# Kernel tuning notes

Measured on AMD Instinct MI355X. Metric: run time of the kernel, lower is better.

The kernel has to match this reference:

```python
import jax, jax.numpy as jnp
import numpy as np

B, T, D = 4, 2048, 1024
E, K, F = 8, 2, 4096


def setup_inputs() -> dict:
    key = jax.random.key(0)
    ks = jax.random.split(key, 6)
    s = 0.02
    return {
        "x": jax.random.normal(ks[0], (B, T, D), dtype=jnp.float32),
        "gate_w": jax.random.normal(ks[1], (D, E), dtype=jnp.float32) * s,
        "w1": jax.random.normal(ks[2], (E, D, F), dtype=jnp.float32) * s,
        "b1": jax.random.normal(ks[3], (E, F), dtype=jnp.float32) * s,
        "w2": jax.random.normal(ks[4], (E, F, D), dtype=jnp.float32) * s,
        "b2": jax.random.normal(ks[5], (E, D), dtype=jnp.float32) * s,
    }


def reference(x, gate_w, w1, b1, w2, b2):
    b, t, d = x.shape
    xf = x.reshape(-1, d)                       # [N, D]
    logits = xf @ gate_w                        # [N, E]
    topv, topi = jax.lax.top_k(logits, K)       # [N, K]
    gates = jax.nn.softmax(topv, axis=-1)       # [N, K]
    # per-token per-expert combine weight (zero for unselected experts)
    onehot = jax.nn.one_hot(topi, E, dtype=xf.dtype)       # [N, K, E]
    comb = jnp.einsum('nk,nke->ne', gates, onehot)          # [N, E]
    out = jnp.zeros_like(xf)
    for e in range(E):  # small fixed expert loop; keeps [N,F] intermediate only
        h = jax.nn.gelu(xf @ w1[e] + b1[e], approximate=False)  # [N, F]
        y = h @ w2[e] + b2[e]                                   # [N, D]
        out = out + comb[:, e:e + 1] * y
    return out.reshape(b, t, d)
```

## Files before the change

kernel.cpp:

```cpp
#include <hip/hip_runtime.h>
#include <stdint.h>
#include <stddef.h>

#define N_TOK 8192
#define DIM   1024
#define NE    8
#define NF    4096
#define TM    128
#define TN    128
#define BKK   64
#define RCAP  (N_TOK*2 + NE*TM)
#define MAXMT (N_TOK/TM)

typedef __attribute__((ext_vector_type(8))) short short8;
typedef __attribute__((ext_vector_type(4))) float f32x4;

__device__ __forceinline__ float bf2f(short s){
  unsigned u = ((unsigned)(unsigned short)s) << 16;
  return __builtin_bit_cast(float, u);
}
__device__ __forceinline__ short f2bf(float f){
  unsigned u = __builtin_bit_cast(unsigned, f);
  u += 0x7fffu + ((u >> 16) & 1u);
  return (short)(u >> 16);
}

#define GLD_LDS16(g, l) __builtin_amdgcn_global_load_lds( \
    (const __attribute__((address_space(1))) void*)(g),   \
    (__attribute__((address_space(3))) void*)(l), 16, 0, 0)

__global__ __launch_bounds__(256) void gate_kernel(
    const float* __restrict__ x, const float* __restrict__ gw,
    int* __restrict__ topi, float* __restrict__ gatev, int* __restrict__ ctrl)
{
  int t = blockIdx.x * 4 + (threadIdx.x >> 6);
  int lane = threadIdx.x & 63;
  const float* xr = x + (size_t)t * DIM;
  float p[NE];
  #pragma unroll
  for (int e = 0; e < NE; e++) p[e] = 0.f;
  for (int i = lane; i < DIM; i += 64){
    float xv = xr[i];
    const float* g = gw + i * NE;
    #pragma unroll
    for (int e = 0; e < NE; e++) p[e] += xv * g[e];
  }
  #pragma unroll
  for (int off = 32; off > 0; off >>= 1){
    #pragma unroll
    for (int e = 0; e < NE; e++) p[e] += __shfl_xor(p[e], off, 64);
  }
  if (lane == 0){
    int i1 = 0; float v1 = p[0];
    #pragma unroll
    for (int e = 1; e < NE; e++) if (p[e] > v1){ v1 = p[e]; i1 = e; }
    int i2 = -1; float v2 = -3.4e38f;
    #pragma unroll
    for (int e = 0; e < NE; e++) if (e != i1 && p[e] > v2){ v2 = p[e]; i2 = e; }
    float ex = expf(v2 - v1);
    float g2 = ex / (1.f + ex);
    float g1 = 1.f - g2;
    topi[t*2]   = i1;  topi[t*2+1]  = i2;
    gatev[t*2]  = g1;  gatev[t*2+1] = g2;
    atomicAdd(&ctrl[i1], 1);
    atomicAdd(&ctrl[i2], 1);
  }
}

__global__ void scan_kernel(int* ctrl){
  if (threadIdx.x == 0){
    int tot = 0;
    for (int e = 0; e < NE; e++){
      int c = ctrl[e];
      int cap = (c + TM - 1) & ~(TM - 1);
      ctrl[16+e] = tot; ctrl[24+e] = cap; tot += cap;
    }
  }
}

__global__ __launch_bounds__(256) void scatter_kernel(
    const int* __restrict__ topi, int* ctrl,
    int* __restrict__ rowTok, int* __restrict__ tok2row)
{
  int t = blockIdx.x * 256 + threadIdx.x;
  #pragma unroll
  for (int k = 0; k < 2; k++){
    int e = topi[t*2 + k];
    int pos = atomicAdd(&ctrl[8+e], 1);
    int r = ctrl[16+e] + pos;
    rowTok[r] = t;
    tok2row[t*2 + k] = r;
  }
}

__global__ void pad_kernel(const int* __restrict__ ctrl, int* __restrict__ rowTok){
  int e = blockIdx.x;
  int cnt = ctrl[e], cap = ctrl[24+e], off = ctrl[16+e];
  for (int i = cnt + threadIdx.x; i < cap; i += blockDim.x)
    rowTok[off + i] = N_TOK;
}

__global__ __launch_bounds__(256) void cast_x_kernel(
    const float* __restrict__ x, short* __restrict__ xb)
{
  size_t i = ((size_t)blockIdx.x * 256 + threadIdx.x) * 8;
  if (i >= (size_t)(N_TOK + 1) * DIM) return;
  short8 o;
  if (i < (size_t)N_TOK * DIM){
    #pragma unroll
    for (int j = 0; j < 8; j++) o[j] = f2bf(x[i + j]);
  } else {
    #pragma unroll
    for (int j = 0; j < 8; j++) o[j] = 0;
  }
  *(short8*)(xb + i) = o;
}

__global__ __launch_bounds__(256) void transpose_cast_kernel(
    const float* __restrict__ src, short* __restrict__ dst, int Kd, int Nd)
{
  __shared__ float Ls[64][65];
  int e = blockIdx.z;
  int k0 = blockIdx.y * 64, n0 = blockIdx.x * 64;
  const float* s = src + (size_t)e * Kd * Nd;
  short*       d = dst + (size_t)e * Kd * Nd;
  int t = threadIdx.x;
  int kr = t >> 4, nc = (t & 15) * 4;
  #pragma unroll
  for (int rr = 0; rr < 4; rr++){
    int k = rr*16 + kr;
    f32x4 v = *(const f32x4*)(s + (size_t)(k0 + k) * Nd + n0 + nc);
    Ls[k][nc+0] = v[0]; Ls[k][nc+1] = v[1];
    Ls[k][nc+2] = v[2]; Ls[k][nc+3] = v[3];
  }
  __syncthreads();
  int nr = t >> 2, kc = (t & 3) * 16;
  short o[16];
  #pragma unroll
  for (int i = 0; i < 16; i++) o[i] = f2bf(Ls[kc + i][nr]);
  short* dp = d + (size_t)(n0 + nr) * Kd + k0 + kc;
  *(short8*)(dp)     = *(short8*)&o[0];
  *(short8*)(dp + 8) = *(short8*)&o[8];
}

__global__ __launch_bounds__(256) void ffn1_kernel(
    const short* __restrict__ Xb, const short* __restrict__ W1t,
    const float* __restrict__ b1, const int* __restrict__ ctrl,
    const int* __restrict__ rowTok, short* __restrict__ H)
{
  int e = blockIdx.z, mt = blockIdx.y, nb = blockIdx.x;
  int cap = ctrl[24+e];
  if (mt * TM >= cap) return;
  int rowbase = ctrl[16+e] + mt * TM;

  __shared__ __align__(16) short As[TM][BKK];
  __shared__ __align__(16) short Bs[TN][BKK];

  int tid = threadIdx.x, w = tid >> 6, lane = tid & 63;
  int rsub = lane >> 3, ksub = lane & 7;
  int sw = (ksub ^ rsub) * 8;

  const short* ap[4];
  #pragma unroll
  for (int j = 0; j < 4; j++){
    int g = rowTok[rowbase + w*32 + j*8 + rsub];
    ap[j] = Xb + (size_t)g * DIM + sw;
  }
  const short* bbase = W1t + ((size_t)e * NF + (size_t)nb * TN) * DIM;
  const short* bp[4];
  #pragma unroll
  for (int j = 0; j < 4; j++)
    bp[j] = bbase + (size_t)((w*4 + j)*8 + rsub) * DIM + sw;

  char* AsB = (char*)As; char* BsB = (char*)Bs;
  int ml = lane & 15, q = lane >> 4;
  int wm = w & 1, wn = w >> 1;
  int mx = ml & 7;
  const short8* Ar = (const short8*)As;
  const short8* Br = (const short8*)Bs;

  f32x4 acc[4][4];
  #pragma unroll
  for (int i = 0; i < 4; i++){
    #pragma unroll
    for (int j = 0; j < 4; j++){ f32x4 z = {0.f,0.f,0.f,0.f}; acc[i][j] = z; }
  }

  for (int kb = 0; kb < DIM/BKK; kb++){
    #pragma unroll
    for (int j = 0; j < 4; j++) GLD_LDS16(ap[j] + kb*BKK, AsB + (w*4 + j)*1024);
    #pragma unroll
    for (int j = 0; j < 4; j++) GLD_LDS16(bp[j] + kb*BKK, BsB + (w*4 + j)*1024);
    __syncthreads();
    #pragma unroll
    for (int ks = 0; ks < 2; ks++){
      int c = (ks*4 + q) ^ mx;
      short8 a[4], b[4];
      #pragma unroll
      for (int mi = 0; mi < 4; mi++) a[mi] = Ar[(wm*64 + mi*16 + ml)*8 + c];
      #pragma unroll
      for (int ni = 0; ni < 4; ni++) b[ni] = Br[(wn*64 + ni*16 + ml)*8 + c];
      #pragma unroll
      for (int mi = 0; mi < 4; mi++){
        #pragma unroll
        for (int ni = 0; ni < 4; ni++)
          acc[mi][ni] = __builtin_amdgcn_mfma_f32_16x16x32_bf16(a[mi], b[ni], acc[mi][ni], 0, 0, 0);
      }
    }
    __syncthreads();
  }

  #pragma unroll
  for (int ni = 0; ni < 4; ni++){
    int f = nb*TN + wn*64 + ni*16 + ml;
    float bb = b1[e*NF + f];
    #pragma unroll
    for (int mi = 0; mi < 4; mi++){
      #pragma unroll
      for (int r = 0; r < 4; r++){
        int m = wm*64 + mi*16 + q*4 + r;
        float v = acc[mi][ni][r] + bb;
        float h = 0.5f * v * (1.f + erff(v * 0.70710678118654752f));
        H[(size_t)(rowbase + m) * NF + f] = f2bf(h);
      }
    }
  }
}

__global__ __launch_bounds__(256) void ffn2_kernel(
    const short* __restrict__ H, const short* __restrict__ W2t,
    const float* __restrict__ b2, const int* __restrict__ ctrl,
    short* __restrict__ Yp)
{
  int e = blockIdx.z, mt = blockIdx.y, nb = blockIdx.x;
  int cap = ctrl[24+e];
  if (mt * TM >= cap) return;
  int rowbase = ctrl[16+e] + mt * TM;

  __shared__ __align__(16) short As[TM][BKK];
  __shared__ __align__(16) short Bs[TN][BKK];

  int tid = threadIdx.x, w = tid >> 6, lane = tid & 63;
  int rsub = lane >> 3, ksub = lane & 7;
  int sw = (ksub ^ rsub) * 8;

  const short* ap[4];
  #pragma unroll
  for (int j = 0; j < 4; j++){
    int r = rowbase + w*32 + j*8 + rsub;
    ap[j] = H + (size_t)r * NF + sw;
  }
  const short* bbase = W2t + ((size_t)e * DIM + (size_t)nb * TN) * NF;
  const short* bp[4];
  #pragma unroll
  for (int j = 0; j < 4; j++)
    bp[j] = bbase + (size_t)((w*4 + j)*8 + rsub) * NF + sw;

  char* AsB = (char*)As; char* BsB = (char*)Bs;
  int ml = lane & 15, q = lane >> 4;
  int wm = w & 1, wn = w >> 1;
  int mx = ml & 7;
  const short8* Ar = (const short8*)As;
  const short8* Br = (const short8*)Bs;

  f32x4 acc[4][4];
  #pragma unroll
  for (int i = 0; i < 4; i++){
    #pragma unroll
    for (int j = 0; j < 4; j++){ f32x4 z = {0.f,0.f,0.f,0.f}; acc[i][j] = z; }
  }

  for (int kb = 0; kb < NF/BKK; kb++){
    #pragma unroll
    for (int j = 0; j < 4; j++) GLD_LDS16(ap[j] + kb*BKK, AsB + (w*4 + j)*1024);
    #pragma unroll
    for (int j = 0; j < 4; j++) GLD_LDS16(bp[j] + kb*BKK, BsB + (w*4 + j)*1024);
    __syncthreads();
    #pragma unroll
    for (int ks = 0; ks < 2; ks++){
      int c = (ks*4 + q) ^ mx;
      short8 a[4], b[4];
      #pragma unroll
      for (int mi = 0; mi < 4; mi++) a[mi] = Ar[(wm*64 + mi*16 + ml)*8 + c];
      #pragma unroll
      for (int ni = 0; ni < 4; ni++) b[ni] = Br[(wn*64 + ni*16 + ml)*8 + c];
      #pragma unroll
      for (int mi = 0; mi < 4; mi++){
        #pragma unroll
        for (int ni = 0; ni < 4; ni++)
          acc[mi][ni] = __builtin_amdgcn_mfma_f32_16x16x32_bf16(a[mi], b[ni], acc[mi][ni], 0, 0, 0);
      }
    }
    __syncthreads();
  }

  #pragma unroll
  for (int ni = 0; ni < 4; ni++){
    int d = nb*TN + wn*64 + ni*16 + ml;
    float bb = b2[e*DIM + d];
    #pragma unroll
    for (int mi = 0; mi < 4; mi++){
      #pragma unroll
      for (int r = 0; r < 4; r++){
        int m = wm*64 + mi*16 + q*4 + r;
        Yp[(size_t)(rowbase + m) * DIM + d] = f2bf(acc[mi][ni][r] + bb);
      }
    }
  }
}

__global__ __launch_bounds__(256) void combine_kernel(
    const short* __restrict__ Yp, const int* __restrict__ tok2row,
    const float* __restrict__ gatev, float* __restrict__ out)
{
  int idx = blockIdx.x * 256 + threadIdx.x;
  int t = idx >> 7, d8 = idx & 127;
  int r0 = tok2row[t*2], r1 = tok2row[t*2 + 1];
  float g0 = gatev[t*2], g1 = gatev[t*2 + 1];
  short8 y0 = *(const short8*)(Yp + (size_t)r0 * DIM + d8*8);
  short8 y1 = *(const short8*)(Yp + (size_t)r1 * DIM + d8*8);
  float o[8];
  #pragma unroll
  for (int j = 0; j < 8; j++) o[j] = g0 * bf2f(y0[j]) + g1 * bf2f(y1[j]);
  f32x4 v0 = {o[0], o[1], o[2], o[3]};
  f32x4 v1 = {o[4], o[5], o[6], o[7]};
  f32x4* dst = (f32x4*)(out + (size_t)t * DIM + d8*8);
  dst[0] = v0; dst[1] = v1;
}

extern "C" void kernel_launch(void* const* d_in, const int* in_sizes, int n_in,
                              void* d_out, int out_size, void* d_ws, size_t ws_size,
                              hipStream_t stream)
{
  const float* x  = (const float*)d_in[0];
  const float* gw = (const float*)d_in[1];
  const float* w1 = (const float*)d_in[2];
  const float* b1 = (const float*)d_in[3];
  const float* w2 = (const float*)d_in[4];
  const float* b2 = (const float*)d_in[5];
  float* out = (float*)d_out;

  char* ws = (char*)d_ws;
  size_t o = 0;
  int*   ctrl    = (int*)(ws + o); o += 256;
  int*   topi    = (int*)(ws + o); o += (size_t)N_TOK*2*4;
  float* gatev   = (float*)(ws + o); o += (size_t)N_TOK*2*4;
  int*   rowTok  = (int*)(ws + o); o += (size_t)RCAP*4;
  int*   tok2row = (int*)(ws + o); o += (size_t)N_TOK*2*4;
  o = (o + 255) & ~(size_t)255;
  short* Xb  = (short*)(ws + o); o += (size_t)(N_TOK + 1)*DIM*2;
  short* W1t = (short*)(ws + o); o += (size_t)NE*DIM*NF*2;
  short* W2t = (short*)(ws + o); o += (size_t)NE*NF*DIM*2;
  short* H   = (short*)(ws + o); o += (size_t)RCAP*NF*2;
  short* Yp  = (short*)(ws + o); o += (size_t)RCAP*DIM*2;
  (void)in_sizes; (void)n_in; (void)out_size;

  if (o > ws_size) return;

  hipMemsetAsync(ctrl, 0, 256, stream);
  gate_kernel<<<N_TOK/4, 256, 0, stream>>>(x, gw, topi, gatev, ctrl);
  scan_kernel<<<1, 64, 0, stream>>>(ctrl);
  scatter_kernel<<<N_TOK/256, 256, 0, stream>>>(topi, ctrl, rowTok, tok2row);
  pad_kernel<<<NE, 128, 0, stream>>>(ctrl, rowTok);
  cast_x_kernel<<<((N_TOK + 1)*DIM/8 + 255)/256, 256, 0, stream>>>(x, Xb);
  transpose_cast_kernel<<<dim3(NF/64, DIM/64, NE), 256, 0, stream>>>(w1, W1t, DIM, NF);
  transpose_cast_kernel<<<dim3(DIM/64, NF/64, NE), 256, 0, stream>>>(w2, W2t, NF, DIM);
  ffn1_kernel<<<dim3(NF/TN, MAXMT, NE), 256, 0, stream>>>(Xb, W1t, b1, ctrl, rowTok, H);
  ffn2_kernel<<<dim3(DIM/TN, MAXMT, NE), 256, 0, stream>>>(H, W2t, b2, ctrl, Yp);
  combine_kernel<<<N_TOK*(DIM/8)/256, 256, 0, stream>>>(Yp, tok2row, gatev, out);
}
```

Measured before the change: 1.128 ms.

## Double-buffer LDS tiles in FFN GEMMs, remap blocks across XCDs, raise MFMA priority

Both FFN GEMM kernels now use two LDS buffers, so the next K-tile's global-to-LDS load is issued before the MFMAs on the current tile run. This is meant to hide load latency behind compute and leaves one barrier per iteration instead of two. Workgroup IDs are also remapped so consecutive tiles land on the same XCD, which should improve L2 reuse of weights. s_setprio is raised around the MFMA bursts. LDS use doubles to 64KB per block, which may reduce occupancy, and the remap assumes the workgroup count divides evenly by 8.

Result: slower. 1.157 ms (+2.6%).

```diff
diff --git a/kernel.cpp b/kernel.cpp
--- a/kernel.cpp
+++ b/kernel.cpp
@@ -29,6 +29,17 @@
     (const __attribute__((address_space(1))) void*)(g),   \
     (__attribute__((address_space(3))) void*)(l), 16, 0, 0)
 
+__device__ __forceinline__ void xcd_map(int nx, int& nb, int& mt, int& e){
+  int h   = blockIdx.x + nx * (blockIdx.y + MAXMT * blockIdx.z);
+  int nwg = nx * MAXMT * NE;
+  int q   = nwg >> 3;
+  int wk  = (h & 7) * q + (h >> 3);
+  nb = wk % nx;
+  int r = wk / nx;
+  mt = r % MAXMT;
+  e  = r / MAXMT;
+}
+
 __global__ __launch_bounds__(256) void gate_kernel(
     const float* __restrict__ x, const float* __restrict__ gw,
     int* __restrict__ topi, float* __restrict__ gatev, int* __restrict__ ctrl)
@@ -148,13 +159,14 @@
     const float* __restrict__ b1, const int* __restrict__ ctrl,
     const int* __restrict__ rowTok, short* __restrict__ H)
 {
-  int e = blockIdx.z, mt = blockIdx.y, nb = blockIdx.x;
+  int e, mt, nb;
+  xcd_map(NF/TN, nb, mt, e);
   int cap = ctrl[24+e];
   if (mt * TM >= cap) return;
   int rowbase = ctrl[16+e] + mt * TM;
 
-  __shared__ __align__(16) short As[TM][BKK];
-  __shared__ __align__(16) short Bs[TN][BKK];
+  __shared__ __align__(16) short As[2][TM][BKK];
+  __shared__ __align__(16) short Bs[2][TN][BKK];
 
   int tid = threadIdx.x, w = tid >> 6, lane = tid & 63;
   int rsub = lane >> 3, ksub = lane & 7;
@@ -172,12 +184,10 @@
   for (int j = 0; j < 4; j++)
     bp[j] = bbase + (size_t)((w*4 + j)*8 + rsub) * DIM + sw;
 
-  char* AsB = (char*)As; char* BsB = (char*)Bs;
+  char* const AsB = (char*)As; char* const BsB = (char*)Bs;
   int ml = lane & 15, q = lane >> 4;
   int wm = w & 1, wn = w >> 1;
   int mx = ml & 7;
-  const short8* Ar = (const short8*)As;
-  const short8* Br = (const short8*)Bs;
 
   f32x4 acc[4][4];
   #pragma unroll
@@ -186,12 +196,24 @@
     for (int j = 0; j < 4; j++){ f32x4 z = {0.f,0.f,0.f,0.f}; acc[i][j] = z; }
   }
 
+  #pragma unroll
+  for (int j = 0; j < 4; j++) GLD_LDS16(ap[j], AsB + (w*4 + j)*1024);
+  #pragma unroll
+  for (int j = 0; j < 4; j++) GLD_LDS16(bp[j], BsB + (w*4 + j)*1024);
+  __syncthreads();
+
+  int buf = 0;
   for (int kb = 0; kb < DIM/BKK; kb++){
-    #pragma unroll
-    for (int j = 0; j < 4; j++) GLD_LDS16(ap[j] + kb*BKK, AsB + (w*4 + j)*1024);
-    #pragma unroll
-    for (int j = 0; j < 4; j++) GLD_LDS16(bp[j] + kb*BKK, BsB + (w*4 + j)*1024);
-    __syncthreads();
+    if (kb + 1 < DIM/BKK){
+      char* an = AsB + (buf^1)*16384;
+      char* bn = BsB + (buf^1)*16384;
+      #pragma unroll
+      for (int j = 0; j < 4; j++) GLD_LDS16(ap[j] + (kb+1)*BKK, an + (w*4 + j)*1024);
+      #pragma unroll
+      for (int j = 0; j < 4; j++) GLD_LDS16(bp[j] + (kb+1)*BKK, bn + (w*4 + j)*1024);
+    }
+    const short8* Ar = (const short8*)(AsB + buf*16384);
+    const short8* Br = (const short8*)(BsB + buf*16384);
     #pragma unroll
     for (int ks = 0; ks < 2; ks++){
       int c = (ks*4 + q) ^ mx;
@@ -200,14 +222,17 @@
       for (int mi = 0; mi < 4; mi++) a[mi] = Ar[(wm*64 + mi*16 + ml)*8 + c];
       #pragma unroll
       for (int ni = 0; ni < 4; ni++) b[ni] = Br[(wn*64 + ni*16 + ml)*8 + c];
+      __builtin_amdgcn_s_setprio(1);
       #pragma unroll
       for (int mi = 0; mi < 4; mi++){
         #pragma unroll
         for (int ni = 0; ni < 4; ni++)
           acc[mi][ni] = __builtin_amdgcn_mfma_f32_16x16x32_bf16(a[mi], b[ni], acc[mi][ni], 0, 0, 0);
       }
+      __builtin_amdgcn_s_setprio(0);
     }
     __syncthreads();
+    buf ^= 1;
   }
 
   #pragma unroll
@@ -232,13 +257,14 @@
     const float* __restrict__ b2, const int* __restrict__ ctrl,
     short* __restrict__ Yp)
 {
-  int e = blockIdx.z, mt = blockIdx.y, nb = blockIdx.x;
+  int e, mt, nb;
+  xcd_map(DIM/TN, nb, mt, e);
   int cap = ctrl[24+e];
   if (mt * TM >= cap) return;
   int rowbase = ctrl[16+e] + mt * TM;
 
-  __shared__ __align__(16) short As[TM][BKK];
-  __shared__ __align__(16) short Bs[TN][BKK];
+  __shared__ __align__(16) short As[2][TM][BKK];
+  __shared__ __align__(16) short Bs[2][TN][BKK];
 
   int tid = threadIdx.x, w = tid >> 6, lane = tid & 63;
   int rsub = lane >> 3, ksub = lane & 7;
@@ -256,12 +282,10 @@
   for (int j = 0; j < 4; j++)
     bp[j] = bbase + (size_t)((w*4 + j)*8 + rsub) * NF + sw;
 
-  char* AsB = (char*)As; char* BsB = (char*)Bs;
+  char* const AsB = (char*)As; char* const BsB = (char*)Bs;
   int ml = lane & 15, q = lane >> 4;
   int wm = w & 1, wn = w >> 1;
   int mx = ml & 7;
-  const short8* Ar = (const short8*)As;
-  const short8* Br = (const short8*)Bs;
 
   f32x4 acc[4][4];
   #pragma unroll
@@ -270,12 +294,24 @@
     for (int j = 0; j < 4; j++){ f32x4 z = {0.f,0.f,0.f,0.f}; acc[i][j] = z; }
   }
 
+  #pragma unroll
+  for (int j = 0; j < 4; j++) GLD_LDS16(ap[j], AsB + (w*4 + j)*1024);
+  #pragma unroll
+  for (int j = 0; j < 4; j++) GLD_LDS16(bp[j], BsB + (w*4 + j)*1024);
+  __syncthreads();
+
+  int buf = 0;
   for (int kb = 0; kb < NF/BKK; kb++){
-    #pragma unroll
-    for (int j = 0; j < 4; j++) GLD_LDS16(ap[j] + kb*BKK, AsB + (w*4 + j)*1024);
-    #pragma unroll
-    for (int j = 0; j < 4; j++) GLD_LDS16(bp[j] + kb*BKK, BsB + (w*4 + j)*1024);
-    __syncthreads();
+    if (kb + 1 < NF/BKK){
+      char* an = AsB + (buf^1)*16384;
+      char* bn = BsB + (buf^1)*16384;
+      #pragma unroll
+      for (int j = 0; j < 4; j++) GLD_LDS16(ap[j] + (kb+1)*BKK, an + (w*4 + j)*1024);
+      #pragma unroll
+      for (int j = 0; j < 4; j++) GLD_LDS16(bp[j] + (kb+1)*BKK, bn + (w*4 + j)*1024);
+    }
+    const short8* Ar = (const short8*)(AsB + buf*16384);
+    const short8* Br = (const short8*)(BsB + buf*16384);
     #pragma unroll
     for (int ks = 0; ks < 2; ks++){
       int c = (ks*4 + q) ^ mx;
@@ -284,14 +320,17 @@
       for (int mi = 0; mi < 4; mi++) a[mi] = Ar[(wm*64 + mi*16 + ml)*8 + c];
       #pragma unroll
       for (int ni = 0; ni < 4; ni++) b[ni] = Br[(wn*64 + ni*16 + ml)*8 + c];
+      __builtin_amdgcn_s_setprio(1);
       #pragma unroll
       for (int mi = 0; mi < 4; mi++){
         #pragma unroll
         for (int ni = 0; ni < 4; ni++)
           acc[mi][ni] = __builtin_amdgcn_mfma_f32_16x16x32_bf16(a[mi], b[ni], acc[mi][ni], 0, 0, 0);
       }
+      __builtin_amdgcn_s_setprio(0);
     }
     __syncthreads();
+    buf ^= 1;
   }
 
   #pragma unroll
```

## Use compact tile list and XCD-aware block remap for grouped expert GEMMs

Applied to the files above, without the earlier changes.

The scan kernel now emits a compact list of (expert, row-base) tiles, so the FFN kernels launch a 2D grid sized to the real number of M-tiles instead of a padded E×MAXMT grid with many early-exit blocks. A swizzle maps linear block ids so that consecutive work items land on the same XCD, which is meant to improve L2 reuse of weight and activation tiles across blocks. The cost is an extra indirection through small tile tables and a serial loop in the scan kernel.

Measured after the change: 1.117 ms. About the same (-1.0%).

```diff
diff --git a/kernel.cpp b/kernel.cpp
--- a/kernel.cpp
+++ b/kernel.cpp
@@ -10,7 +10,7 @@
 #define TN    128
 #define BKK   64
 #define RCAP  (N_TOK*2 + NE*TM)
-#define MAXMT (N_TOK/TM)
+#define MTL   (N_TOK*2/TM + NE - 1)
 
 typedef __attribute__((ext_vector_type(8))) short short8;
 typedef __attribute__((ext_vector_type(4))) float f32x4;
@@ -28,6 +28,15 @@
 #define GLD_LDS16(g, l) __builtin_amdgcn_global_load_lds( \
     (const __attribute__((address_space(1))) void*)(g),   \
     (__attribute__((address_space(3))) void*)(l), 16, 0, 0)
+
+__device__ __forceinline__ void xcd_map2(int nx, int& nb, int& tt){
+  int h   = blockIdx.x + nx * blockIdx.y;
+  int nwg = nx * MTL;
+  int q   = nwg >> 3;
+  int wk  = (h & 7) * q + (h >> 3);
+  nb = wk % nx;
+  tt = wk / nx;
+}
 
 __global__ __launch_bounds__(256) void gate_kernel(
     const float* __restrict__ x, const float* __restrict__ gw,
@@ -67,14 +76,19 @@
   }
 }
 
-__global__ void scan_kernel(int* ctrl){
+__global__ void scan_kernel(int* ctrl, int* __restrict__ tileE, int* __restrict__ tileR){
   if (threadIdx.x == 0){
-    int tot = 0;
+    int tot = 0, nt = 0;
     for (int e = 0; e < NE; e++){
       int c = ctrl[e];
       int cap = (c + TM - 1) & ~(TM - 1);
-      ctrl[16+e] = tot; ctrl[24+e] = cap; tot += cap;
-    }
+      ctrl[16+e] = tot; ctrl[24+e] = cap;
+      for (int m = 0; m < cap; m += TM){
+        tileE[nt] = e; tileR[nt] = tot + m; nt++;
+      }
+      tot += cap;
+    }
+    ctrl[32] = nt;
   }
 }
 
@@ -146,12 +160,14 @@
 __global__ __launch_bounds__(256) void ffn1_kernel(
     const short* __restrict__ Xb, const short* __restrict__ W1t,
     const float* __restrict__ b1, const int* __restrict__ ctrl,
+    const int* __restrict__ tileE, const int* __restrict__ tileR,
     const int* __restrict__ rowTok, short* __restrict__ H)
 {
-  int e = blockIdx.z, mt = blockIdx.y, nb = blockIdx.x;
-  int cap = ctrl[24+e];
-  if (mt * TM >= cap) return;
-  int rowbase = ctrl[16+e] + mt * TM;
+  int nb, tt;
+  xcd_map2(NF/TN, nb, tt);
+  if (tt >= ctrl[32]) return;
+  int e = tileE[tt];
+  int rowbase = tileR[tt];
 
   __shared__ __align__(16) short As[TM][BKK];
   __shared__ __align__(16) short Bs[TN][BKK];
@@ -230,12 +246,14 @@
 __global__ __launch_bounds__(256) void ffn2_kernel(
     const short* __restrict__ H, const short* __restrict__ W2t,
     const float* __restrict__ b2, const int* __restrict__ ctrl,
+    const int* __restrict__ tileE, const int* __restrict__ tileR,
     short* __restrict__ Yp)
 {
-  int e = blockIdx.z, mt = blockIdx.y, nb = blockIdx.x;
-  int cap = ctrl[24+e];
-  if (mt * TM >= cap) return;
-  int rowbase = ctrl[16+e] + mt * TM;
+  int nb, tt;
+  xcd_map2(DIM/TN, nb, tt);
+  if (tt >= ctrl[32]) return;
+  int e = tileE[tt];
+  int rowbase = tileR[tt];
 
   __shared__ __align__(16) short As[TM][BKK];
   __shared__ __align__(16) short Bs[TN][BKK];
@@ -347,6 +365,8 @@
   float* gatev   = (float*)(ws + o); o += (size_t)N_TOK*2*4;
   int*   rowTok  = (int*)(ws + o); o += (size_t)RCAP*4;
   int*   tok2row = (int*)(ws + o); o += (size_t)N_TOK*2*4;
+  int*   tileE   = (int*)(ws + o); o += 1024;
+  int*   tileR   = (int*)(ws + o); o += 1024;
   o = (o + 255) & ~(size_t)255;
   short* Xb  = (short*)(ws + o); o += (size_t)(N_TOK + 1)*DIM*2;
   short* W1t = (short*)(ws + o); o += (size_t)NE*DIM*NF*2;
@@ -359,13 +379,13 @@
 
   hipMemsetAsync(ctrl, 0, 256, stream);
   gate_kernel<<<N_TOK/4, 256, 0, stream>>>(x, gw, topi, gatev, ctrl);
-  scan_kernel<<<1, 64, 0, stream>>>(ctrl);
+  scan_kernel<<<1, 64, 0, stream>>>(ctrl, tileE, tileR);
   scatter_kernel<<<N_TOK/256, 256, 0, stream>>>(topi, ctrl, rowTok, tok2row);
   pad_kernel<<<NE, 128, 0, stream>>>(ctrl, rowTok);
   cast_x_kernel<<<((N_TOK + 1)*DIM/8 + 255)/256, 256, 0, stream>>>(x, Xb);
   transpose_cast_kernel<<<dim3(NF/64, DIM/64, NE), 256, 0, stream>>>(w1, W1t, DIM, NF);
   transpose_cast_kernel<<<dim3(DIM/64, NF/64, NE), 256, 0, stream>>>(w2, W2t, NF, DIM);
-  ffn1_kernel<<<dim3(NF/TN, MAXMT, NE), 256, 0, stream>>>(Xb, W1t, b1, ctrl, rowTok, H);
-  ffn2_kernel<<<dim3(DIM/TN, MAXMT, NE), 256, 0, stream>>>(H, W2t, b2, ctrl, Yp);
+  ffn1_kernel<<<dim3(NF/TN, MTL), 256, 0, stream>>>(Xb, W1t, b1, ctrl, tileE, tileR, rowTok, H);
+  ffn2_kernel<<<dim3(DIM/TN, MTL), 256, 0, stream>>>(H, W2t, b2, ctrl, tileE, tileR, Yp);
   combine_kernel<<<N_TOK*(DIM/8)/256, 256, 0, stream>>>(Yp, tok2row, gatev, out);
 }
```
